# Optimization experiments

Hardware: AMD Instinct MI355X
Metric: run time of the kernel (lower is better)

## Reference

```python
import jax, jax.numpy as jnp
import numpy as np

FEATURE_DIM = 512
NUM_HEADS = 8
HEAD_DIM = FEATURE_DIM // NUM_HEADS
B, L = 4, 2048


def setup_inputs() -> dict:
    key = jax.random.key(0)
    ks = jax.random.split(key, 10)
    s = 1.0 / np.sqrt(FEATURE_DIM)
    inp = {
        "ppg": jax.random.normal(ks[0], (B, FEATURE_DIM, L), dtype=jnp.float32),
        "ecg": jax.random.normal(ks[1], (B, FEATURE_DIM, L), dtype=jnp.float32),
        "Wq": jax.random.uniform(ks[2], (FEATURE_DIM, FEATURE_DIM), jnp.float32, -s, s),
        "bq": jnp.zeros((FEATURE_DIM,), jnp.float32),
        "Wk": jax.random.uniform(ks[3], (FEATURE_DIM, FEATURE_DIM), jnp.float32, -s, s),
        "bk": jnp.zeros((FEATURE_DIM,), jnp.float32),
        "Wv": jax.random.uniform(ks[4], (FEATURE_DIM, FEATURE_DIM), jnp.float32, -s, s),
        "bv": jnp.zeros((FEATURE_DIM,), jnp.float32),
        "Wo": jax.random.uniform(ks[5], (FEATURE_DIM, FEATURE_DIM), jnp.float32, -s, s),
        "bo": jnp.zeros((FEATURE_DIM,), jnp.float32),
    }
    return inp


def reference(ppg, ecg, Wq, bq, Wk, bk, Wv, bv, Wo, bo):
    # ppg/ecg: (B, C, L) -> (B, L, C)
    x = jnp.transpose(ppg, (0, 2, 1))
    y = jnp.transpose(ecg, (0, 2, 1))
    q = x @ Wq.T + bq  # (B, L, C)
    k = y @ Wk.T + bk
    v = y @ Wv.T + bv
    # split heads: (B, H, L, D)
    def split(t):
        return jnp.transpose(t.reshape(B, L, NUM_HEADS, HEAD_DIM), (0, 2, 1, 3))
    qh, kh, vh = split(q), split(k), split(v)
    scores = jnp.einsum('bhqd,bhkd->bhqk', qh, kh) / jnp.sqrt(jnp.float32(HEAD_DIM))
    probs = jax.nn.softmax(scores, axis=-1)  # dropout is identity in eval mode
    ctx = jnp.einsum('bhqk,bhkd->bhqd', probs, vh)
    ctx = jnp.transpose(ctx, (0, 2, 1, 3)).reshape(B, L, FEATURE_DIM)
    out = ctx @ Wo.T + bo + x  # residual with transposed ppg
    return jnp.transpose(out, (0, 2, 1))  # (B, C, L)
```

## Files before the change

### kernel.cpp

```cpp
#include <hip/hip_runtime.h>
#include <hip/hip_bf16.h>

static constexpr int Bc = 4;
static constexpr int Lc = 2048;
static constexpr int Cc = 512;
static constexpr int Hc = 8;
static constexpr int Dc = 64;

using short8  = __attribute__((ext_vector_type(8))) short;
using float4v = __attribute__((ext_vector_type(4))) float;

static __device__ __forceinline__ unsigned short f2bf(float f) {
    __hip_bfloat16 h = __float2bfloat16(f);
    return *reinterpret_cast<unsigned short*>(&h);
}

__global__ __launch_bounds__(256) void prep_kernel(
    const float* __restrict__ ppg, const float* __restrict__ ecg,
    const float* __restrict__ Wq, const float* __restrict__ Wk,
    const float* __restrict__ Wv, const float* __restrict__ Wo,
    unsigned short* __restrict__ Xt_ppg, unsigned short* __restrict__ Xt_ecg,
    unsigned short* __restrict__ Wbf)
{
    __shared__ float Ts[64 * 69];
    const int task = blockIdx.x;
    const int tid  = threadIdx.x;

    if (task < 2048) {
        const int src = task >> 10;
        const int rem = task & 1023;
        const int b   = rem >> 8;
        const int c0  = ((rem >> 5) & 7) * 64;
        const int l0  = (rem & 31) * 64;
        const float* X = src ? ecg : ppg;
        unsigned short* Xt = src ? Xt_ecg : Xt_ppg;

        #pragma unroll
        for (int j = 0; j < 4; ++j) {
            int idx = tid + j * 256;
            int c = idx >> 4, l4 = idx & 15;
            float4 v = *(const float4*)(X + ((size_t)b * Cc + c0 + c) * Lc + l0 + l4 * 4);
            Ts[c * 69 + l4 * 4 + 0] = v.x;
            Ts[c * 69 + l4 * 4 + 1] = v.y;
            Ts[c * 69 + l4 * 4 + 2] = v.z;
            Ts[c * 69 + l4 * 4 + 3] = v.w;
        }
        __syncthreads();
        #pragma unroll
        for (int j = 0; j < 8; ++j) {
            int u = tid + j * 256;
            int l = u >> 5, p2 = u & 31;
            float a = Ts[(2 * p2) * 69 + l];
            float bb = Ts[(2 * p2 + 1) * 69 + l];
            ushort2 pk; pk.x = f2bf(a); pk.y = f2bf(bb);
            *(ushort2*)(Xt + ((size_t)b * Lc + l0 + l) * Cc + c0 + 2 * p2) = pk;
        }
    } else {
        const int wb   = task - 2048;
        const int widx = wb >> 7;
        const float* W = widx == 0 ? Wq : widx == 1 ? Wk : widx == 2 ? Wv : Wo;
        size_t off = (size_t)(wb & 127) * 2048 + (size_t)tid * 8;
        float4 v0 = *(const float4*)(W + off);
        float4 v1 = *(const float4*)(W + off + 4);
        unsigned short pk[8] = {f2bf(v0.x), f2bf(v0.y), f2bf(v0.z), f2bf(v0.w),
                                f2bf(v1.x), f2bf(v1.y), f2bf(v1.z), f2bf(v1.w)};
        *(short8*)(Wbf + (size_t)widx * Cc * Cc + off) = *(const short8*)pk;
    }
}

__global__ __launch_bounds__(256) void proj_kernel(
    const unsigned short* __restrict__ Xt_ppg,
    const unsigned short* __restrict__ Xt_ecg,
    const unsigned short* __restrict__ Wbf,
    const float* __restrict__ bq, const float* __restrict__ bk,
    const float* __restrict__ bv,
    unsigned short* __restrict__ Qw, unsigned short* __restrict__ Kw,
    unsigned short* __restrict__ Vtw)
{
    constexpr int LDW = 72;
    const int z = blockIdx.z, p = z >> 2, b = z & 3;
    const int l0 = blockIdx.x * 128, n0 = blockIdx.y * 64;
    const unsigned short* X = (p == 0) ? Xt_ppg : Xt_ecg;
    const unsigned short* W = Wbf + (size_t)p * Cc * Cc;
    const float* bias = (p == 0) ? bq : (p == 1) ? bk : bv;

    const int tid = threadIdx.x, wave = tid >> 6, lane = tid & 63;
    const int l16 = lane & 15, quad = lane >> 4;

    __shared__ __align__(16) unsigned short At[128 * LDW];
    __shared__ __align__(16) unsigned short Bt[64 * LDW];

    float4v acc[8] = {};
    short8 areg[4], breg[2];

    const int arow = tid >> 3, ac8 = tid & 7;
    #pragma unroll
    for (int j = 0; j < 4; ++j)
        areg[j] = *(const short8*)(X + ((size_t)b * Lc + l0 + arow + j * 32) * Cc + ac8 * 8);
    #pragma unroll
    for (int j = 0; j < 2; ++j)
        breg[j] = *(const short8*)(W + (size_t)(n0 + arow + j * 32) * Cc + ac8 * 8);

    for (int c0 = 0; c0 < Cc; c0 += 64) {
        #pragma unroll
        for (int j = 0; j < 4; ++j)
            *(short8*)&At[(arow + j * 32) * LDW + ac8 * 8] = areg[j];
        #pragma unroll
        for (int j = 0; j < 2; ++j)
            *(short8*)&Bt[(arow + j * 32) * LDW + ac8 * 8] = breg[j];
        __syncthreads();

        if (c0 + 64 < Cc) {
            #pragma unroll
            for (int j = 0; j < 4; ++j)
                areg[j] = *(const short8*)(X + ((size_t)b * Lc + l0 + arow + j * 32) * Cc
                                           + c0 + 64 + ac8 * 8);
            #pragma unroll
            for (int j = 0; j < 2; ++j)
                breg[j] = *(const short8*)(W + (size_t)(n0 + arow + j * 32) * Cc
                                           + c0 + 64 + ac8 * 8);
        }

        if (p < 2) {
            #pragma unroll
            for (int ks = 0; ks < 2; ++ks) {
                #pragma unroll
                for (int lt = 0; lt < 2; ++lt) {
                    short8 af = *(const short8*)&At[(wave * 32 + lt * 16 + l16) * LDW
                                                    + ks * 32 + quad * 8];
                    #pragma unroll
                    for (int t = 0; t < 4; ++t) {
                        short8 bf = *(const short8*)&Bt[(t * 16 + l16) * LDW
                                                        + ks * 32 + quad * 8];
                        acc[lt * 4 + t] = __builtin_amdgcn_mfma_f32_16x16x32_bf16(
                            af, bf, acc[lt * 4 + t], 0, 0, 0);
                    }
                }
            }
        } else {
            #pragma unroll
            for (int ks = 0; ks < 2; ++ks) {
                short8 af = *(const short8*)&Bt[(wave * 16 + l16) * LDW
                                                + ks * 32 + quad * 8];
                #pragma unroll
                for (int t = 0; t < 8; ++t) {
                    short8 bf = *(const short8*)&At[(t * 16 + l16) * LDW
                                                    + ks * 32 + quad * 8];
                    acc[t] = __builtin_amdgcn_mfma_f32_16x16x32_bf16(
                        af, bf, acc[t], 0, 0, 0);
                }
            }
        }
        __syncthreads();
    }

    const int h = n0 >> 6;
    const int bh = b * Hc + h;

    if (p < 2) {
        const float sc = (p == 0) ? 0.18033688011112042f : 1.0f;
        unsigned short* dst = (p == 0) ? Qw : Kw;
        #pragma unroll
        for (int lt = 0; lt < 2; ++lt) {
            #pragma unroll
            for (int t = 0; t < 4; ++t) {
                float bia = bias[n0 + t * 16 + l16];
                #pragma unroll
                for (int r = 0; r < 4; ++r) {
                    int l = l0 + wave * 32 + lt * 16 + quad * 4 + r;
                    dst[((size_t)bh * Lc + l) * Dc + t * 16 + l16] =
                        f2bf((acc[lt * 4 + t][r] + bia) * sc);
                }
            }
        }
    } else {
        #pragma unroll
        for (int t = 0; t < 8; ++t) {
            #pragma unroll
            for (int r = 0; r < 4; ++r) {
                int d = wave * 16 + quad * 4 + r;
                float bia = bias[n0 + d];
                int l = l0 + t * 16 + l16;
                Vtw[((size_t)bh * Dc + d) * Lc + l] = f2bf(acc[t][r] + bia);
            }
        }
    }
}

__global__ __launch_bounds__(256) void attn_mfma_kernel(
    const unsigned short* __restrict__ Qg,
    const unsigned short* __restrict__ Kg,
    const unsigned short* __restrict__ Vtg,
    unsigned short* __restrict__ ctx)
{
    constexpr int LDW = 72;
    const int bh   = blockIdx.y;
    const int q0   = blockIdx.x * 64;
    const int tid  = threadIdx.x;
    const int wave = tid >> 6;
    const int lane = tid & 63;
    const int l16  = lane & 15;
    const int quad = lane >> 4;

    __shared__ __align__(16) unsigned short Kt[64 * LDW];
    __shared__ __align__(16) unsigned short Vt[64 * LDW];
    __shared__ __align__(16) unsigned short PT[64 * LDW];

    const int srow = tid >> 3, sc8 = tid & 7;

    const unsigned short* Qb = Qg + ((size_t)bh * Lc + q0) * Dc;
    #pragma unroll
    for (int j = 0; j < 2; ++j)
        *(short8*)&PT[(srow + j * 32) * LDW + sc8 * 8] =
            *(const short8*)(Qb + (srow + j * 32) * Dc + sc8 * 8);
    __syncthreads();

    short8 qf[2];
    #pragma unroll
    for (int ks = 0; ks < 2; ++ks)
        qf[ks] = *(const short8*)&PT[(wave * 16 + l16) * LDW + ks * 32 + quad * 8];

    float4v O[4] = {};
    float lsum = 0.0f;

    const unsigned short* Kb0 = Kg + (size_t)bh * Lc * Dc;
    const unsigned short* Vb0 = Vtg + (size_t)bh * (Dc * Lc);

    short8 kreg[2], vreg[2];
    #pragma unroll
    for (int j = 0; j < 2; ++j) {
        kreg[j] = *(const short8*)(Kb0 + (size_t)(srow + j * 32) * Dc + sc8 * 8);
        vreg[j] = *(const short8*)(Vb0 + (size_t)(srow + j * 32) * Lc + sc8 * 8);
    }

    for (int kc = 0; kc < Lc; kc += 64) {
        #pragma unroll
        for (int j = 0; j < 2; ++j) {
            *(short8*)&Kt[(srow + j * 32) * LDW + sc8 * 8] = kreg[j];
            *(short8*)&Vt[(srow + j * 32) * LDW + sc8 * 8] = vreg[j];
        }
        __syncthreads();

        if (kc + 64 < Lc) {
            #pragma unroll
            for (int j = 0; j < 2; ++j) {
                kreg[j] = *(const short8*)(Kb0 + (size_t)(kc + 64 + srow + j * 32) * Dc
                                           + sc8 * 8);
                vreg[j] = *(const short8*)(Vb0 + (size_t)(srow + j * 32) * Lc
                                           + kc + 64 + sc8 * 8);
            }
        }

        float4v S[4];
        #pragma unroll
        for (int kt = 0; kt < 4; ++kt) S[kt] = (float4v){0.f, 0.f, 0.f, 0.f};
        #pragma unroll
        for (int ks = 0; ks < 2; ++ks) {
            #pragma unroll
            for (int kt = 0; kt < 4; ++kt) {
                short8 af = *(const short8*)&Kt[(kt * 16 + l16) * LDW
                                                + ks * 32 + quad * 8];
                S[kt] = __builtin_amdgcn_mfma_f32_16x16x32_bf16(
                    af, qf[ks], S[kt], 0, 0, 0);
            }
        }

        #pragma unroll
        for (int kt = 0; kt < 4; ++kt) {
            float p0 = __builtin_amdgcn_exp2f(S[kt][0]);
            float p1 = __builtin_amdgcn_exp2f(S[kt][1]);
            float p2 = __builtin_amdgcn_exp2f(S[kt][2]);
            float p3 = __builtin_amdgcn_exp2f(S[kt][3]);
            lsum += (p0 + p1) + (p2 + p3);
            ushort4 pk;
            pk.x = f2bf(p0); pk.y = f2bf(p1); pk.z = f2bf(p2); pk.w = f2bf(p3);
            *(ushort4*)&PT[(wave * 16 + l16) * LDW + kt * 16 + quad * 4] = pk;
        }

        #pragma unroll
        for (int ks = 0; ks < 2; ++ks) {
            short8 pf = *(const short8*)&PT[(wave * 16 + l16) * LDW
                                            + ks * 32 + quad * 8];
            #pragma unroll
            for (int dt = 0; dt < 4; ++dt) {
                short8 vf = *(const short8*)&Vt[(dt * 16 + l16) * LDW
                                                + ks * 32 + quad * 8];
                O[dt] = __builtin_amdgcn_mfma_f32_16x16x32_bf16(
                    vf, pf, O[dt], 0, 0, 0);
            }
        }
        __syncthreads();
    }

    float t = lsum;
    t += __shfl_xor(t, 16, 64);
    t += __shfl_xor(t, 32, 64);
    const float inv_l = 1.0f / t;

    const int b = bh >> 3, h = bh & 7;
    const int q = q0 + wave * 16 + l16;
    #pragma unroll
    for (int dt = 0; dt < 4; ++dt) {
        ushort4 pk;
        pk.x = f2bf(O[dt][0] * inv_l);
        pk.y = f2bf(O[dt][1] * inv_l);
        pk.z = f2bf(O[dt][2] * inv_l);
        pk.w = f2bf(O[dt][3] * inv_l);
        *(ushort4*)(ctx + ((size_t)b * Lc + q) * Cc
                    + h * Dc + dt * 16 + quad * 4) = pk;
    }
}

__global__ __launch_bounds__(256) void outproj_kernel(
    const unsigned short* __restrict__ ctx, const unsigned short* __restrict__ Wo_bf,
    const float* __restrict__ bo, const float* __restrict__ ppg,
    float* __restrict__ out)
{
    constexpr int LDW = 72;
    const int b = blockIdx.z;
    const int l0 = blockIdx.x * 64, n0 = blockIdx.y * 64;
    const int tid = threadIdx.x, wave = tid >> 6, lane = tid & 63;
    const int l16 = lane & 15, quad = lane >> 4;

    __shared__ __align__(16) unsigned short At[64 * LDW];
    __shared__ __align__(16) unsigned short Bt[64 * LDW];

    float4v acc[4] = {};

    for (int c0 = 0; c0 < Cc; c0 += 64) {
        #pragma unroll
        for (int j = 0; j < 2; ++j) {
            int e = tid + j * 256;
            int row = e >> 3, c8 = e & 7;
            *(short8*)&At[row * LDW + c8 * 8] =
                *(const short8*)(Wo_bf + (size_t)(n0 + row) * Cc + c0 + c8 * 8);
            *(short8*)&Bt[row * LDW + c8 * 8] =
                *(const short8*)(ctx + ((size_t)b * Lc + l0 + row) * Cc + c0 + c8 * 8);
        }
        __syncthreads();

        #pragma unroll
        for (int ks = 0; ks < 2; ++ks) {
            short8 af = *(const short8*)&At[(wave * 16 + l16) * LDW + ks * 32 + quad * 8];
            #pragma unroll
            for (int t = 0; t < 4; ++t) {
                short8 bf = *(const short8*)&Bt[(t * 16 + l16) * LDW + ks * 32 + quad * 8];
                acc[t] = __builtin_amdgcn_mfma_f32_16x16x32_bf16(af, bf, acc[t], 0, 0, 0);
            }
        }
        __syncthreads();
    }

    #pragma unroll
    for (int t = 0; t < 4; ++t) {
        #pragma unroll
        for (int r = 0; r < 4; ++r) {
            int n = n0 + wave * 16 + quad * 4 + r;
            int l = l0 + t * 16 + l16;
            size_t oidx = ((size_t)b * Cc + n) * Lc + l;
            out[oidx] = acc[t][r] + bo[n] + ppg[oidx];
        }
    }
}

extern "C" void kernel_launch(void* const* d_in, const int* in_sizes, int n_in,
                              void* d_out, int out_size, void* d_ws, size_t ws_size,
                              hipStream_t stream) {
    const float* ppg = (const float*)d_in[0];
    const float* ecg = (const float*)d_in[1];
    const float* Wq  = (const float*)d_in[2];
    const float* bq  = (const float*)d_in[3];
    const float* Wk  = (const float*)d_in[4];
    const float* bk  = (const float*)d_in[5];
    const float* Wv  = (const float*)d_in[6];
    const float* bv  = (const float*)d_in[7];
    const float* Wo  = (const float*)d_in[8];
    const float* bo  = (const float*)d_in[9];
    float* out = (float*)d_out;

    const size_t plane = (size_t)Bc * Lc * Cc;
    unsigned short* Xt_ppg = (unsigned short*)d_ws;
    unsigned short* Xt_ecg = Xt_ppg + plane;
    unsigned short* Wbf    = Xt_ecg + plane;
    unsigned short* Qw     = Wbf + (size_t)4 * Cc * Cc;
    unsigned short* Kw     = Qw + plane;
    unsigned short* Vtw    = Kw + plane;
    unsigned short* ctx    = Vtw + plane;

    prep_kernel<<<2560, 256, 0, stream>>>(ppg, ecg, Wq, Wk, Wv, Wo,
                                          Xt_ppg, Xt_ecg, Wbf);

    dim3 g1(Lc / 128, Cc / 64, 3 * Bc);
    proj_kernel<<<g1, 256, 0, stream>>>(Xt_ppg, Xt_ecg, Wbf, bq, bk, bv,
                                        Qw, Kw, Vtw);

    dim3 g2(Lc / 64, Bc * Hc);
    attn_mfma_kernel<<<g2, 256, 0, stream>>>(Qw, Kw, Vtw, ctx);

    dim3 g3(Lc / 64, Cc / 64, Bc);
    outproj_kernel<<<g3, 256, 0, stream>>>(ctx, Wbf + (size_t)3 * Cc * Cc,
                                           bo, ppg, out);
}
```

Measured before the change: 194.1 us.

## Enlarge GEMM tiles in projection and output-projection kernels, add register prefetch

The QKV projection now uses 128x128 tiles with a 2x2 wave layout, giving 16 accumulators per wave. The output projection uses 64x128 tiles, and its global loads are staged through registers so the next K-slice loads while the current one computes. The aim is more MFMA work per shared-memory load and fewer global loads per output, with memory latency hidden in outproj. In exchange, register and LDS use go up and fewer blocks are launched, which may lower occupancy.

```diff
diff --git a/kernel.cpp b/kernel.cpp
--- a/kernel.cpp
+++ b/kernel.cpp
@@ -79,109 +79,102 @@
 {
     constexpr int LDW = 72;
     const int z = blockIdx.z, p = z >> 2, b = z & 3;
-    const int l0 = blockIdx.x * 128, n0 = blockIdx.y * 64;
+    const int l0 = blockIdx.x * 128, n0 = blockIdx.y * 128;
     const unsigned short* X = (p == 0) ? Xt_ppg : Xt_ecg;
     const unsigned short* W = Wbf + (size_t)p * Cc * Cc;
     const float* bias = (p == 0) ? bq : (p == 1) ? bk : bv;
 
     const int tid = threadIdx.x, wave = tid >> 6, lane = tid & 63;
     const int l16 = lane & 15, quad = lane >> 4;
+    const int wr = wave >> 1, wc = wave & 1;
 
     __shared__ __align__(16) unsigned short At[128 * LDW];
-    __shared__ __align__(16) unsigned short Bt[64 * LDW];
-
-    float4v acc[8] = {};
-    short8 areg[4], breg[2];
-
-    const int arow = tid >> 3, ac8 = tid & 7;
-    #pragma unroll
-    for (int j = 0; j < 4; ++j)
-        areg[j] = *(const short8*)(X + ((size_t)b * Lc + l0 + arow + j * 32) * Cc + ac8 * 8);
-    #pragma unroll
-    for (int j = 0; j < 2; ++j)
-        breg[j] = *(const short8*)(W + (size_t)(n0 + arow + j * 32) * Cc + ac8 * 8);
+    __shared__ __align__(16) unsigned short Bt[128 * LDW];
+
+    float4v acc[4][4] = {};
+    short8 areg[4], breg[4];
+
+    const int srow = tid >> 3, sc8 = tid & 7;
+    #pragma unroll
+    for (int j = 0; j < 4; ++j) {
+        areg[j] = *(const short8*)(X + ((size_t)b * Lc + l0 + srow + j * 32) * Cc + sc8 * 8);
+        breg[j] = *(const short8*)(W + (size_t)(n0 + srow + j * 32) * Cc + sc8 * 8);
+    }
 
     for (int c0 = 0; c0 < Cc; c0 += 64) {
         #pragma unroll
-        for (int j = 0; j < 4; ++j)
-            *(short8*)&At[(arow + j * 32) * LDW + ac8 * 8] = areg[j];
-        #pragma unroll
-        for (int j = 0; j < 2; ++j)
-            *(short8*)&Bt[(arow + j * 32) * LDW + ac8 * 8] = breg[j];
+        for (int j = 0; j < 4; ++j) {
+            *(short8*)&At[(srow + j * 32) * LDW + sc8 * 8] = areg[j];
+            *(short8*)&Bt[(srow + j * 32) * LDW + sc8 * 8] = breg[j];
+        }
         __syncthreads();
 
         if (c0 + 64 < Cc) {
             #pragma unroll
-            for (int j = 0; j < 4; ++j)
-                areg[j] = *(const short8*)(X + ((size_t)b * Lc + l0 + arow + j * 32) * Cc
-                                           + c0 + 64 + ac8 * 8);
-            #pragma unroll
-            for (int j = 0; j < 2; ++j)
-                breg[j] = *(const short8*)(W + (size_t)(n0 + arow + j * 32) * Cc
-                                           + c0 + 64 + ac8 * 8);
-        }
-
-        if (p < 2) {
-            #pragma unroll
-            for (int ks = 0; ks < 2; ++ks) {
-                #pragma unroll
-                for (int lt = 0; lt < 2; ++lt) {
-                    short8 af = *(const short8*)&At[(wave * 32 + lt * 16 + l16) * LDW
-                                                    + ks * 32 + quad * 8];
-                    #pragma unroll
-                    for (int t = 0; t < 4; ++t) {
-                        short8 bf = *(const short8*)&Bt[(t * 16 + l16) * LDW
-                                                        + ks * 32 + quad * 8];
-                        acc[lt * 4 + t] = __builtin_amdgcn_mfma_f32_16x16x32_bf16(
-                            af, bf, acc[lt * 4 + t], 0, 0, 0);
-                    }
-                }
-            }
-        } else {
-            #pragma unroll
-            for (int ks = 0; ks < 2; ++ks) {
-                short8 af = *(const short8*)&Bt[(wave * 16 + l16) * LDW
+            for (int j = 0; j < 4; ++j) {
+                areg[j] = *(const short8*)(X + ((size_t)b * Lc + l0 + srow + j * 32) * Cc
+                                           + c0 + 64 + sc8 * 8);
+                breg[j] = *(const short8*)(W + (size_t)(n0 + srow + j * 32) * Cc
+                                           + c0 + 64 + sc8 * 8);
+            }
+        }
+
+        const unsigned short* Am = (p < 2) ? At : Bt;
+        const unsigned short* Bm = (p < 2) ? Bt : At;
+
+        #pragma unroll
+        for (int ks = 0; ks < 2; ++ks) {
+            short8 bf[4];
+            #pragma unroll
+            for (int nt = 0; nt < 4; ++nt)
+                bf[nt] = *(const short8*)&Bm[(wc * 64 + nt * 16 + l16) * LDW
+                                             + ks * 32 + quad * 8];
+            #pragma unroll
+            for (int mt = 0; mt < 4; ++mt) {
+                short8 af = *(const short8*)&Am[(wr * 64 + mt * 16 + l16) * LDW
                                                 + ks * 32 + quad * 8];
                 #pragma unroll
-                for (int t = 0; t < 8; ++t) {
-                    short8 bf = *(const short8*)&At[(t * 16 + l16) * LDW
-                                                    + ks * 32 + quad * 8];
-                    acc[t] = __builtin_amdgcn_mfma_f32_16x16x32_bf16(
-                        af, bf, acc[t], 0, 0, 0);
-                }
-            }
-        }
-        __syncthreads();
-    }
-
-    const int h = n0 >> 6;
-    const int bh = b * Hc + h;
+                for (int nt = 0; nt < 4; ++nt)
+                    acc[mt][nt] = __builtin_amdgcn_mfma_f32_16x16x32_bf16(
+                        af, bf[nt], acc[mt][nt], 0, 0, 0);
+            }
+        }
+        __syncthreads();
+    }
 
     if (p < 2) {
         const float sc = (p == 0) ? 0.18033688011112042f : 1.0f;
         unsigned short* dst = (p == 0) ? Qw : Kw;
         #pragma unroll
-        for (int lt = 0; lt < 2; ++lt) {
-            #pragma unroll
-            for (int t = 0; t < 4; ++t) {
-                float bia = bias[n0 + t * 16 + l16];
+        for (int nt = 0; nt < 4; ++nt) {
+            int n = n0 + wc * 64 + nt * 16 + l16;
+            int h = n >> 6, d = n & 63;
+            int bh = b * Hc + h;
+            float bia = bias[n];
+            #pragma unroll
+            for (int mt = 0; mt < 4; ++mt) {
                 #pragma unroll
                 for (int r = 0; r < 4; ++r) {
-                    int l = l0 + wave * 32 + lt * 16 + quad * 4 + r;
-                    dst[((size_t)bh * Lc + l) * Dc + t * 16 + l16] =
-                        f2bf((acc[lt * 4 + t][r] + bia) * sc);
+                    int l = l0 + wr * 64 + mt * 16 + quad * 4 + r;
+                    dst[((size_t)bh * Lc + l) * Dc + d] =
+                        f2bf((acc[mt][nt][r] + bia) * sc);
                 }
             }
         }
     } else {
         #pragma unroll
-        for (int t = 0; t < 8; ++t) {
+        for (int mt = 0; mt < 4; ++mt) {
             #pragma unroll
             for (int r = 0; r < 4; ++r) {
-                int d = wave * 16 + quad * 4 + r;
-                float bia = bias[n0 + d];
-                int l = l0 + t * 16 + l16;
-                Vtw[((size_t)bh * Dc + d) * Lc + l] = f2bf(acc[t][r] + bia);
+                int n = n0 + wr * 64 + mt * 16 + quad * 4 + r;
+                int h = n >> 6, d = n & 63;
+                int bh = b * Hc + h;
+                float bia = bias[n];
+                #pragma unroll
+                for (int nt = 0; nt < 4; ++nt) {
+                    int l = l0 + wc * 64 + nt * 16 + l16;
+                    Vtw[((size_t)bh * Dc + d) * Lc + l] = f2bf(acc[mt][nt][r] + bia);
+                }
             }
         }
     }
@@ -318,47 +311,76 @@
 {
     constexpr int LDW = 72;
     const int b = blockIdx.z;
-    const int l0 = blockIdx.x * 64, n0 = blockIdx.y * 64;
+    const int l0 = blockIdx.x * 128, n0 = blockIdx.y * 64;
     const int tid = threadIdx.x, wave = tid >> 6, lane = tid & 63;
     const int l16 = lane & 15, quad = lane >> 4;
 
     __shared__ __align__(16) unsigned short At[64 * LDW];
-    __shared__ __align__(16) unsigned short Bt[64 * LDW];
-
-    float4v acc[4] = {};
+    __shared__ __align__(16) unsigned short Bt[128 * LDW];
+
+    float4v acc[4][2] = {};
+    short8 areg[2], breg[4];
+
+    const int srow = tid >> 3, sc8 = tid & 7;
+    #pragma unroll
+    for (int j = 0; j < 2; ++j)
+        areg[j] = *(const short8*)(Wo_bf + (size_t)(n0 + srow + j * 32) * Cc + sc8 * 8);
+    #pragma unroll
+    for (int j = 0; j < 4; ++j)
+        breg[j] = *(const short8*)(ctx + ((size_t)b * Lc + l0 + srow + j * 32) * Cc + sc8 * 8);
 
     for (int c0 = 0; c0 < Cc; c0 += 64) {
         #pragma unroll
-        for (int j = 0; j < 2; ++j) {
-            int e = tid + j * 256;
-            int row = e >> 3, c8 = e & 7;
-            *(short8*)&At[row * LDW + c8 * 8] =
-                *(const short8*)(Wo_bf + (size_t)(n0 + row) * Cc + c0 + c8 * 8);
-            *(short8*)&Bt[row * LDW + c8 * 8] =
-                *(const short8*)(ctx + ((size_t)b * Lc + l0 + row) * Cc + c0 + c8 * 8);
-        }
-        __syncthreads();
+        for (int j = 0; j < 2; ++j)
+            *(short8*)&At[(srow + j * 32) * LDW + sc8 * 8] = areg[j];
+        #pragma unroll
+        for (int j = 0; j < 4; ++j)
+            *(short8*)&Bt[(srow + j * 32) * LDW + sc8 * 8] = breg[j];
+        __syncthreads();
+
+        if (c0 + 64 < Cc) {
+            #pragma unroll
+            for (int j = 0; j < 2; ++j)
+                areg[j] = *(const short8*)(Wo_bf + (size_t)(n0 + srow + j * 32) * Cc
+                                           + c0 + 64 + sc8 * 8);
+            #pragma unroll
+            for (int j = 0; j < 4; ++j)
+                breg[j] = *(const short8*)(ctx + ((size_t)b * Lc + l0 + srow + j * 32) * Cc
+                                           + c0 + 64 + sc8 * 8);
+        }
 
         #pragma unroll
         for (int ks = 0; ks < 2; ++ks) {
-            short8 af = *(const short8*)&At[(wave * 16 + l16) * LDW + ks * 32 + quad * 8];
-            #pragma unroll
-            for (int t = 0; t < 4; ++t) {
-                short8 bf = *(const short8*)&Bt[(t * 16 + l16) * LDW + ks * 32 + quad * 8];
-                acc[t] = __builtin_amdgcn_mfma_f32_16x16x32_bf16(af, bf, acc[t], 0, 0, 0);
-            }
-        }
-        __syncthreads();
-    }
-
-    #pragma unroll
-    for (int t = 0; t < 4; ++t) {
+            short8 bf[2];
+            #pragma unroll
+            for (int nt = 0; nt < 2; ++nt)
+                bf[nt] = *(const short8*)&Bt[(wave * 32 + nt * 16 + l16) * LDW
+                                             + ks * 32 + quad * 8];
+            #pragma unroll
+            for (int mt = 0; mt < 4; ++mt) {
+                short8 af = *(const short8*)&At[(mt * 16 + l16) * LDW
+                                                + ks * 32 + quad * 8];
+                #pragma unroll
+                for (int nt = 0; nt < 2; ++nt)
+                    acc[mt][nt] = __builtin_amdgcn_mfma_f32_16x16x32_bf16(
+                        af, bf[nt], acc[mt][nt], 0, 0, 0);
+            }
+        }
+        __syncthreads();
+    }
+
+    #pragma unroll
+    for (int mt = 0; mt < 4; ++mt) {
         #pragma unroll
         for (int r = 0; r < 4; ++r) {
-            int n = n0 + wave * 16 + quad * 4 + r;
-            int l = l0 + t * 16 + l16;
-            size_t oidx = ((size_t)b * Cc + n) * Lc + l;
-            out[oidx] = acc[t][r] + bo[n] + ppg[oidx];
+            int n = n0 + mt * 16 + quad * 4 + r;
+            float bia = bo[n];
+            #pragma unroll
+            for (int nt = 0; nt < 2; ++nt) {
+                int l = l0 + wave * 32 + nt * 16 + l16;
+                size_t oidx = ((size_t)b * Cc + n) * Lc + l;
+                out[oidx] = acc[mt][nt][r] + bia + ppg[oidx];
+            }
         }
     }
 }
@@ -390,14 +412,14 @@
     prep_kernel<<<2560, 256, 0, stream>>>(ppg, ecg, Wq, Wk, Wv, Wo,
                                           Xt_ppg, Xt_ecg, Wbf);
 
-    dim3 g1(Lc / 128, Cc / 64, 3 * Bc);
+    dim3 g1(Lc / 128, Cc / 128, 3 * Bc);
     proj_kernel<<<g1, 256, 0, stream>>>(Xt_ppg, Xt_ecg, Wbf, bq, bk, bv,
                                         Qw, Kw, Vtw);
 
     dim3 g2(Lc / 64, Bc * Hc);
     attn_mfma_kernel<<<g2, 256, 0, stream>>>(Qw, Kw, Vtw, ctx);
 
-    dim3 g3(Lc / 64, Cc / 64, Bc);
+    dim3 g3(Lc / 128, Cc / 64, Bc);
     outproj_kernel<<<g3, 256, 0, stream>>>(ctx, Wbf + (size_t)3 * Cc * Cc,
                                            bo, ppg, out);
 }
```

Measured after the change: 193.9 us. No clear change (-0.1%).
